# Kernel optimization log

Hardware: AMD Instinct MI355X
Metric: run time of the kernel (lower is better)

## Reference

```python
import jax, jax.numpy as jnp
import numpy as np

B, S, H = 8, 2048, 512
M = 4096
TEMP = 0.1
EPS = 1e-6


def setup_inputs() -> dict:
    key = jax.random.key(0)
    ks = jax.random.split(key, 8)
    scale = 1.0 / np.sqrt(H)
    return {
        "hidden_states": jax.random.normal(ks[0], (B, S, H), dtype=jnp.float32),
        "memory_keys": jax.random.normal(ks[1], (M, H), dtype=jnp.float32),
        "memory_values": jax.random.normal(ks[2], (M, H), dtype=jnp.float32),
        "Wk": jax.random.normal(ks[3], (H, H), dtype=jnp.float32) * scale,
        "bk": jnp.zeros((H,), dtype=jnp.float32),
        "Wo": jax.random.normal(ks[4], (H, H), dtype=jnp.float32) * scale,
        "bo": jnp.zeros((H,), dtype=jnp.float32),
        "memory_usage": jax.random.randint(ks[5], (M,), 0, 2, dtype=jnp.int32),
    }


def reference(hidden_states, memory_keys, memory_values, Wk, bk, Wo, bo, memory_usage):
    # key projection: [B,S,H]
    q = jnp.einsum("bsh,kh->bsk", hidden_states, Wk) + bk
    # L2-style normalization with eps inside rsqrt (matches torch.rsqrt(norm_sq + 1e-6))
    q_n = q * jax.lax.rsqrt(jnp.sum(q * q, axis=-1, keepdims=True) + EPS)
    mk_n = memory_keys * jax.lax.rsqrt(
        jnp.sum(memory_keys * memory_keys, axis=-1, keepdims=True) + EPS
    )
    # cosine-similarity scores over the memory bank: [B,S,M]
    scores = jnp.einsum("bsk,mk->bsm", q_n, mk_n) / TEMP
    mask = (memory_usage > 0).astype(scores.dtype)  # [M]
    scores = scores * mask + (-1e9) * (1.0 - mask)
    attn = jax.nn.softmax(scores, axis=-1)  # [B,S,M]
    retrieved = jnp.einsum("bsm,mv->bsv", attn, memory_values)  # [B,S,H]
    out = jnp.einsum("bsv,hv->bsh", retrieved, Wo) + bo
    return out
```

## Files before the change

### kernel.cpp

```cpp
#include <hip/hip_runtime.h>
#include <cstdint>
#include <cstddef>

#define H_DIM   512
#define M_DIM   4096

typedef unsigned short u16;
typedef short bf16x8 __attribute__((ext_vector_type(8)));
typedef float f32x4  __attribute__((ext_vector_type(4)));

__device__ __forceinline__ u16 f2b(float f) {
  union { float f; uint32_t u; } v; v.f = f;
  uint32_t u = v.u + (0x7FFFu + ((v.u >> 16) & 1u));
  return (u16)(u >> 16);
}

__device__ __forceinline__ bf16x8 cvt8(const float4& lo, const float4& hi) {
  union { u16 u[8]; bf16x8 v; } o;
  o.u[0] = f2b(lo.x); o.u[1] = f2b(lo.y); o.u[2] = f2b(lo.z); o.u[3] = f2b(lo.w);
  o.u[4] = f2b(hi.x); o.u[5] = f2b(hi.y); o.u[6] = f2b(hi.z); o.u[7] = f2b(hi.w);
  return o.v;
}

__global__ void k_f2bf_ww(const float* __restrict__ wk, const float* __restrict__ wo,
                          u16* __restrict__ owk, u16* __restrict__ owo) {
  int i = blockIdx.x * blockDim.x + threadIdx.x;
  const float* src = (i < 65536) ? wk : wo;
  u16* dst = (i < 65536) ? owk : owo;
  int j = i & 65535;
  float4 v = ((const float4*)src)[j];
  ushort4 o;
  o.x = f2b(v.x); o.y = f2b(v.y); o.z = f2b(v.z); o.w = f2b(v.w);
  ((ushort4*)dst)[j] = o;
}

__global__ void k_compact(const int* __restrict__ usage, int* __restrict__ idx,
                          int* __restrict__ meta) {
  __shared__ int cnt[256];
  int t = threadIdx.x;
  int base = t * 16;
  int c = 0;
  #pragma unroll
  for (int i = 0; i < 16; ++i) c += (usage[base + i] > 0) ? 1 : 0;
  cnt[t] = c;
  __syncthreads();
  for (int d = 1; d < 256; d <<= 1) {
    int v = (t >= d) ? cnt[t - d] : 0;
    __syncthreads();
    cnt[t] += v;
    __syncthreads();
  }
  int pos = cnt[t] - c;
  for (int i = 0; i < 16; ++i)
    if (usage[base + i] > 0) idx[pos++] = base + i;
  if (t == 0) {
    int total = cnt[255];
    int keff = ((total + 127) >> 7) << 7;
    meta[0] = total; meta[1] = keff; meta[2] = keff >> 5; meta[3] = keff >> 7;
  }
}

__global__ void k_gather_keys(const float* __restrict__ keys,
                              const int* __restrict__ idx, const int* __restrict__ meta,
                              u16* __restrict__ okeys) {
  int j    = blockIdx.x * 4 + (threadIdx.x >> 6);
  int lane = threadIdx.x & 63;
  int count = meta[0];
  ushort4* kp = (ushort4*)(okeys + (size_t)j * H_DIM);
  if (j >= count) {
    ushort4 z = {0, 0, 0, 0};
    kp[lane] = z; kp[lane + 64] = z;
    return;
  }
  int src = idx[j];
  const float4* rp = (const float4*)(keys + (size_t)src * H_DIM);
  float4 a = rp[lane];
  float4 b = rp[lane + 64];
  float ss = a.x*a.x + a.y*a.y + a.z*a.z + a.w*a.w
           + b.x*b.x + b.y*b.y + b.z*b.z + b.w*b.w;
  #pragma unroll
  for (int d = 1; d < 64; d <<= 1) ss += __shfl_xor(ss, d, 64);
  float s = rsqrtf(ss + 1e-6f);
  ushort4 oa, ob;
  oa.x = f2b(a.x*s); oa.y = f2b(a.y*s); oa.z = f2b(a.z*s); oa.w = f2b(a.w*s);
  ob.x = f2b(b.x*s); ob.y = f2b(b.y*s); ob.z = f2b(b.z*s); ob.w = f2b(b.w*s);
  kp[lane]      = oa;
  kp[lane + 64] = ob;
}

__global__ void k_reduce_l(const float* __restrict__ lpart, float* __restrict__ linv,
                           const int* __restrict__ meta) {
  int r = blockIdx.x * blockDim.x + threadIdx.x;
  int n = meta[1] >> 6;
  float s = 0.0f;
  for (int i = 0; i < n; ++i) s += lpart[(size_t)r * 64 + i];
  linv[r] = 1.0f / s;
}

__global__ __launch_bounds__(256, 3)
void k_gemm_mw(const u16* __restrict__ A, const float* __restrict__ Bf,
               const int* __restrict__ idx, const int* __restrict__ meta,
               u16* __restrict__ outh) {
  __shared__ u16 Ah[2][128 * 32];
  __shared__ u16 Bh[2][128 * 32];

  const int tid  = threadIdx.x;
  const int wave = tid >> 6, lane = tid & 63;
  const int wr = (wave >> 1) * 64;
  const int wc = (wave & 1) * 64;

  const int count = meta[0];
  if (blockIdx.x >= (meta[1] >> 7)) return;
  const int row0 = blockIdx.y << 7;
  const int col0 = blockIdx.x << 7;
  const int kiters = 512 >> 5;

  const int srow   = lane & 15;
  const int schunk = lane >> 4;
  const int lds_off = schunk * 128 + srow * 8;

  const int fr = lane & 15;
  const int fbase = (lane >> 4) * 128 + fr * 8;
  const int g = lane >> 4;

  const char* Ac = (const char*)A;

  uint32_t aB[2];
  uint32_t bB[2];
  bool bval[2];
  #pragma unroll
  for (int s2 = 0; s2 < 2; ++s2) {
    aB[s2] = (uint32_t)(((size_t)(row0 + (wave + s2 * 4) * 16 + srow) * 512u
                         + (size_t)(schunk * 8)) * 2u);
    int mrow = col0 + (wave + s2 * 4) * 16 + srow;
    bval[s2] = (mrow < count);
    int src = bval[s2] ? idx[mrow] : 0;
    bB[s2] = (uint32_t)(((size_t)src * 512u + (size_t)(schunk * 8)) * 4u);
  }

  f32x4 acc[4][4];
  const f32x4 z = {0.0f, 0.0f, 0.0f, 0.0f};
  #pragma unroll
  for (int i = 0; i < 4; ++i)
    #pragma unroll
    for (int j = 0; j < 4; ++j) acc[i][j] = z;

  bf16x8 rA[2];
  float4 rBlo[2], rBhi[2];
  auto gload = [&](int k0) {
    const uint32_t kb  = (uint32_t)(k0 << 1);
    const uint32_t kbf = (uint32_t)(k0 << 2);
    #pragma unroll
    for (int s2 = 0; s2 < 2; ++s2) rA[s2] = *(const bf16x8*)(Ac + aB[s2] + kb);
    #pragma unroll
    for (int s2 = 0; s2 < 2; ++s2) {
      rBlo[s2] = *(const float4*)((const char*)Bf + bB[s2] + kbf);
      rBhi[s2] = *(const float4*)((const char*)Bf + bB[s2] + kbf + 16);
    }
  };

  const float4 zf = {0.f, 0.f, 0.f, 0.f};
  gload(0);
  for (int it = 0; it < kiters; ++it) {
    const int cur = it & 1;
    #pragma unroll
    for (int s2 = 0; s2 < 2; ++s2)
      *(bf16x8*)&Ah[cur][(wave + s2 * 4) * 512 + lds_off] = rA[s2];
    #pragma unroll
    for (int s2 = 0; s2 < 2; ++s2)
      *(bf16x8*)&Bh[cur][(wave + s2 * 4) * 512 + lds_off] =
          bval[s2] ? cvt8(rBlo[s2], rBhi[s2]) : cvt8(zf, zf);
    if (it + 1 < kiters) gload((it + 1) << 5);
    __syncthreads();

    bf16x8 af[4], bfv[4];
    #pragma unroll
    for (int i = 0; i < 4; ++i)
      af[i] = *(const bf16x8*)&Ah[cur][((wr >> 4) + i) * 512 + fbase];
    #pragma unroll
    for (int j = 0; j < 4; ++j)
      bfv[j] = *(const bf16x8*)&Bh[cur][((wc >> 4) + j) * 512 + fbase];
    #pragma unroll
    for (int i = 0; i < 4; ++i)
      #pragma unroll
      for (int j = 0; j < 4; ++j)
        acc[i][j] = __builtin_amdgcn_mfma_f32_16x16x32_bf16(af[i], bfv[j], acc[i][j], 0, 0, 0);
  }

  #pragma unroll
  for (int i = 0; i < 4; ++i) {
    #pragma unroll
    for (int r = 0; r < 4; ++r) {
      int grow = row0 + wr + i * 16 + g * 4 + r;
      #pragma unroll
      for (int j = 0; j < 4; ++j) {
        int gcol = col0 + wc + j * 16 + fr;
        outh[(size_t)grow * (size_t)M_DIM + gcol] = f2b(acc[i][j][r]);
      }
    }
  }
}

#define EPI2_P     0
#define EPI2_OUT   1
#define EPI2_QPROJ 2

template<int EPI>
__global__ __launch_bounds__(512, 2)
void k_gemm2(const u16* __restrict__ A, const u16* __restrict__ B,
             const int* __restrict__ meta,
             float* __restrict__ outf, u16* __restrict__ outh,
             const float* __restrict__ bias,
             float* __restrict__ aux,
             const float* __restrict__ rowscale) {
  constexpr int BM   = (EPI == EPI2_P) ? 256 : 128;
  constexpr int MF   = BM / 32;
  constexpr int NF   = 4;
  constexpr int APS  = BM / 128;
  constexpr int NLA  = BM / 64;
  constexpr int NLB  = 4;
  constexpr int ASUB = BM * 32;
  constexpr int BSUB = 256 * 32;
  constexpr bool BF32 = (EPI == EPI2_QPROJ);

  __shared__ u16 Ah[2][BM * 64];
  __shared__ u16 Bh[2][256 * 64];

  const int tid  = threadIdx.x;
  const int wave = tid >> 6, lane = tid & 63;
  const int wave_m = wave >> 2, wave_n = wave & 3;
  const int wm0 = wave_m * (BM >> 1);
  const int wn0 = wave_n * 64;
  const int fr  = lane & 15, g = lane >> 4;
  const int fbase = g * 128 + fr * 8;

  int m0, r0, kel;
  if (EPI == EPI2_P) {
    int id = blockIdx.x + (blockIdx.y << 4);
    int xcd = id & 7, s = id >> 3;
    r0 = (xcd * 8 + (s >> 4)) << 8;
    m0 = (s & 15) << 8;
    if (m0 >= meta[1]) return;
    kel = 512;
  } else if (EPI == EPI2_OUT) {
    int id = blockIdx.x + (blockIdx.y << 2);
    int xcd = id & 7, s = id >> 3;
    r0 = (xcd * 8 + (s >> 2)) << 8;
    m0 = (s & 3) << 7;
    kel = meta[1];
  } else {
    int id = blockIdx.x + (blockIdx.y << 2);
    int xcd = id & 7, s = id >> 3;
    r0 = (xcd * 8 + (s >> 2)) << 8;
    m0 = (s & 3) << 7;
    kel = 512;
  }
  const int kiters = kel >> 6;
  if (kiters <= 0) return;
  const int kstr = (EPI == EPI2_OUT) ? M_DIM : 512;

  const char* Ac = (const char*)A;
  const char* Bc = (const char*)B;
  uint32_t aB[NLA], bB[NLB];
  #pragma unroll
  for (int s2 = 0; s2 < NLA; ++s2) {
    int ks = s2 / APS;
    int u  = tid + (s2 % APS) * 512;
    int row = ((u >> 6) << 4) + (u & 15);
    int kch = (u >> 4) & 3;
    aB[s2] = (uint32_t)(((size_t)(m0 + row) * (size_t)kstr
                         + (size_t)(ks * 32 + kch * 8)) * 2u);
  }
  #pragma unroll
  for (int s2 = 0; s2 < NLB; ++s2) {
    int ks = s2 >> 1;
    int u  = tid + (s2 & 1) * 512;
    int row = ((u >> 6) << 4) + (u & 15);
    int kch = (u >> 4) & 3;
    bB[s2] = (uint32_t)(((size_t)(r0 + row) * (size_t)kstr
                         + (size_t)(ks * 32 + kch * 8)) * (BF32 ? 4u : 2u));
  }

  f32x4 acc[MF][NF];
  const f32x4 z = {0.0f, 0.0f, 0.0f, 0.0f};
  #pragma unroll
  for (int i = 0; i < MF; ++i)
    #pragma unroll
    for (int j = 0; j < NF; ++j) acc[i][j] = z;

  auto gloadA = [&](bf16x8 (&ra)[NLA], int it1) {
    const uint32_t kb = (uint32_t)(it1 << 7);
    #pragma unroll
    for (int s2 = 0; s2 < NLA; ++s2) ra[s2] = *(const bf16x8*)(Ac + aB[s2] + kb);
  };
  auto gloadBh = [&](bf16x8 (&rb)[NLB], int it1) {
    const uint32_t kb = (uint32_t)(it1 << 7);
    #pragma unroll
    for (int s2 = 0; s2 < NLB; ++s2) rb[s2] = *(const bf16x8*)(Bc + bB[s2] + kb);
  };
  auto gloadBf = [&](float4 (&lo)[NLB], float4 (&hi)[NLB], int it1) {
    const uint32_t kb = (uint32_t)(it1 << 8);
    #pragma unroll
    for (int s2 = 0; s2 < NLB; ++s2) {
      lo[s2] = *(const float4*)(Bc + bB[s2] + kb);
      hi[s2] = *(const float4*)(Bc + bB[s2] + kb + 16);
    }
  };
  auto commitA = [&](int cur, bf16x8 (&ra)[NLA]) {
    #pragma unroll
    for (int s2 = 0; s2 < NLA; ++s2)
      *(bf16x8*)&Ah[cur][(s2 / APS) * ASUB + (tid + (s2 % APS) * 512) * 8] = ra[s2];
  };
  auto commitBh = [&](int cur, bf16x8 (&rb)[NLB]) {
    #pragma unroll
    for (int s2 = 0; s2 < NLB; ++s2)
      *(bf16x8*)&Bh[cur][(s2 >> 1) * BSUB + (tid + (s2 & 1) * 512) * 8] = rb[s2];
  };
  auto commitBf = [&](int cur, float4 (&lo)[NLB], float4 (&hi)[NLB]) {
    #pragma unroll
    for (int s2 = 0; s2 < NLB; ++s2)
      *(bf16x8*)&Bh[cur][(s2 >> 1) * BSUB + (tid + (s2 & 1) * 512) * 8] =
          cvt8(lo[s2], hi[s2]);
  };
  auto compute = [&](int cur) {
    bf16x8 af[MF], bfv[NF];
    #pragma unroll
    for (int i = 0; i < MF; ++i)
      af[i] = *(const bf16x8*)&Ah[cur][((wm0 >> 4) + i) * 512 + fbase];
    #pragma unroll
    for (int j = 0; j < NF; ++j)
      bfv[j] = *(const bf16x8*)&Bh[cur][((wn0 >> 4) + j) * 512 + fbase];
    #pragma unroll
    for (int i = 0; i < MF; ++i)
      #pragma unroll
      for (int j = 0; j < NF; ++j)
        acc[i][j] = __builtin_amdgcn_mfma_f32_16x16x32_bf16(af[i], bfv[j], acc[i][j], 0, 0, 0);
    #pragma unroll
    for (int i = 0; i < MF; ++i)
      af[i] = *(const bf16x8*)&Ah[cur][ASUB + ((wm0 >> 4) + i) * 512 + fbase];
    #pragma unroll
    for (int j = 0; j < NF; ++j)
      bfv[j] = *(const bf16x8*)&Bh[cur][BSUB + ((wn0 >> 4) + j) * 512 + fbase];
    #pragma unroll
    for (int i = 0; i < MF; ++i)
      #pragma unroll
      for (int j = 0; j < NF; ++j)
        acc[i][j] = __builtin_amdgcn_mfma_f32_16x16x32_bf16(af[i], bfv[j], acc[i][j], 0, 0, 0);
  };

  if constexpr (EPI == EPI2_P) {
    bf16x8 rA[NLA], rB[NLB];
    gloadA(rA, 0); gloadBh(rB, 0);
    for (int it = 0; it < kiters; ++it) {
      const int cur = it & 1;
      commitA(cur, rA); commitBh(cur, rB);
      if (it + 1 < kiters) { gloadA(rA, it + 1); gloadBh(rB, it + 1); }
      __syncthreads();
      compute(cur);
    }
  } else if constexpr (!BF32) {
    bf16x8 a0[NLA], b0[NLB], a1[NLA], b1[NLB];
    gloadA(a0, 0); gloadBh(b0, 0);
    if (kiters > 1) { gloadA(a1, 1); gloadBh(b1, 1); }
    for (int it = 0; it < kiters; it += 2) {
      commitA(0, a0); commitBh(0, b0);
      if (it + 2 < kiters) { gloadA(a0, it + 2); gloadBh(b0, it + 2); }
      __syncthreads();
      compute(0);
      commitA(1, a1); commitBh(1, b1);
      if (it + 3 < kiters) { gloadA(a1, it + 3); gloadBh(b1, it + 3); }
      __syncthreads();
      compute(1);
    }
  } else {
    bf16x8 a0[NLA], a1[NLA];
    float4 b0lo[NLB], b0hi[NLB], b1lo[NLB], b1hi[NLB];
    gloadA(a0, 0); gloadBf(b0lo, b0hi, 0);
    if (kiters > 1) { gloadA(a1, 1); gloadBf(b1lo, b1hi, 1); }
    for (int it = 0; it < kiters; it += 2) {
      commitA(0, a0); commitBf(0, b0lo, b0hi);
      if (it + 2 < kiters) { gloadA(a0, it + 2); gloadBf(b0lo, b0hi, it + 2); }
      __syncthreads();
      compute(0);
      commitA(1, a1); commitBf(1, b1lo, b1hi);
      if (it + 3 < kiters) { gloadA(a1, it + 3); gloadBf(b1lo, b1hi, it + 3); }
      __syncthreads();
      compute(1);
    }
  }

  if (EPI == EPI2_P) {
    const int count = meta[0];
    float rq10[NF];
    #pragma unroll
    for (int j = 0; j < NF; ++j) {
      const size_t rr = (size_t)(r0 + wn0 + j * 16 + fr);
      float ssum = 0.0f;
      #pragma unroll
      for (int i = 0; i < 8; ++i) ssum += rowscale[rr * 8 + i];
      rq10[j] = rsqrtf(ssum + 1e-6f) * 10.0f;
    }
    float sj[NF] = {0.f, 0.f, 0.f, 0.f};
    #pragma unroll
    for (int i = 0; i < MF; ++i) {
      const int mb = m0 + wm0 + i * 16 + g * 4;
      #pragma unroll
      for (int j = 0; j < NF; ++j) {
        const size_t rr = (size_t)(r0 + wn0 + j * 16 + fr);
        float p0 = (mb + 0 < count) ? __expf(acc[i][j][0] * rq10[j]) : 0.0f;
        float p1 = (mb + 1 < count) ? __expf(acc[i][j][1] * rq10[j]) : 0.0f;
        float p2 = (mb + 2 < count) ? __expf(acc[i][j][2] * rq10[j]) : 0.0f;
        float p3 = (mb + 3 < count) ? __expf(acc[i][j][3] * rq10[j]) : 0.0f;
        ushort4 st; st.x = f2b(p0); st.y = f2b(p1); st.z = f2b(p2); st.w = f2b(p3);
        *(ushort4*)(outh + rr * M_DIM + mb) = st;
        sj[j] += (p0 + p1) + (p2 + p3);
      }
    }
    const int slot = (m0 + wm0) >> 6;
    #pragma unroll
    for (int j = 0; j < NF; ++j) {
      float s = sj[j];
      s += __shfl_xor(s, 16, 64);
      s += __shfl_xor(s, 32, 64);
      if (lane < 16) {
        const size_t rr = (size_t)(r0 + wn0 + j * 16 + lane);
        aux[rr * 64 + slot]     = s;
        aux[rr * 64 + slot + 1] = 0.0f;
      }
    }
  } else if (EPI == EPI2_OUT) {
    float scl[NF];
    #pragma unroll
    for (int j = 0; j < NF; ++j)
      scl[j] = rowscale[r0 + wn0 + j * 16 + fr];
    #pragma unroll
    for (int i = 0; i < MF; ++i) {
      const int hb = m0 + wm0 + i * 16 + g * 4;
      const float4 bv = *(const float4*)(bias + hb);
      #pragma unroll
      for (int j = 0; j < NF; ++j) {
        const size_t rr = (size_t)(r0 + wn0 + j * 16 + fr);
        float4 o;
        o.x = acc[i][j][0] * scl[j] + bv.x;
        o.y = acc[i][j][1] * scl[j] + bv.y;
        o.z = acc[i][j][2] * scl[j] + bv.z;
        o.w = acc[i][j][3] * scl[j] + bv.w;
        *(float4*)(outf + rr * H_DIM + hb) = o;
      }
    }
  } else {
    float sj[NF] = {0.f, 0.f, 0.f, 0.f};
    #pragma unroll
    for (int i = 0; i < MF; ++i) {
      const int kb = m0 + wm0 + i * 16 + g * 4;
      const float4 bkv = *(const float4*)(bias + kb);
      #pragma unroll
      for (int j = 0; j < NF; ++j) {
        const size_t rr = (size_t)(r0 + wn0 + j * 16 + fr);
        float v0 = acc[i][j][0] + bkv.x;
        float v1 = acc[i][j][1] + bkv.y;
        float v2 = acc[i][j][2] + bkv.z;
        float v3 = acc[i][j][3] + bkv.w;
        ushort4 st; st.x = f2b(v0); st.y = f2b(v1); st.z = f2b(v2); st.w = f2b(v3);
        *(ushort4*)(outh + rr * H_DIM + kb) = st;
        sj[j] += v0 * v0 + v1 * v1 + v2 * v2 + v3 * v3;
      }
    }
    const int slot = (m0 + wm0) >> 6;
    #pragma unroll
    for (int j = 0; j < NF; ++j) {
      float s = sj[j];
      s += __shfl_xor(s, 16, 64);
      s += __shfl_xor(s, 32, 64);
      if (lane < 16)
        aux[(size_t)(r0 + wn0 + j * 16 + lane) * 8 + slot] = s;
    }
  }
}

extern "C" void kernel_launch(void* const* d_in, const int* in_sizes, int n_in,
                              void* d_out, int out_size, void* d_ws, size_t ws_size,
                              hipStream_t stream) {
  const float* hidden = (const float*)d_in[0];
  const float* mkeys  = (const float*)d_in[1];
  const float* mvals  = (const float*)d_in[2];
  const float* Wk     = (const float*)d_in[3];
  const float* bk     = (const float*)d_in[4];
  const float* Wo     = (const float*)d_in[5];
  const float* bo     = (const float*)d_in[6];
  const int*   usage  = (const int*)d_in[7];
  (void)in_sizes; (void)n_in; (void)out_size; (void)ws_size;

  char* ws = (char*)d_ws;
  int*   idx   = (int*)(ws + 0);
  int*   meta  = (int*)(ws + 16384);
  float* lpart = (float*)(ws + 1048576);
  float* qss   = (float*)(ws + 5242880);
  u16*   wkb   = (u16*)(ws + 16777216);
  u16*   wob   = (u16*)(ws + 17301504);
  u16*   mkn   = (u16*)(ws + 17825792);
  u16*   qb    = (u16*)(ws + 26214400);
  u16*   MWt   = (u16*)(ws + 42991616);
  u16*   P     = (u16*)(ws + 47185920);
  float* linv  = (float*)(ws + 183828480);

  k_f2bf_ww<<<512, 256, 0, stream>>>(Wk, Wo, wkb, wob);

  k_compact<<<1, 256, 0, stream>>>(usage, idx, meta);
  k_gather_keys<<<1024, 256, 0, stream>>>(mkeys, idx, meta, mkn);

  k_gemm2<EPI2_QPROJ><<<dim3(4, 64), 512, 0, stream>>>(wkb, (const u16*)hidden,
      nullptr, nullptr, qb, bk, qss, nullptr);

  k_gemm_mw<<<dim3(16, 4), 256, 0, stream>>>(wob, mvals, idx, meta, MWt);

  k_gemm2<EPI2_P><<<dim3(16, 64), 512, 0, stream>>>(mkn, qb, meta,
      nullptr, P, nullptr, lpart, qss);
  k_reduce_l<<<64, 256, 0, stream>>>(lpart, linv, meta);

  k_gemm2<EPI2_OUT><<<dim3(4, 64), 512, 0, stream>>>(MWt, P, meta,
      (float*)d_out, nullptr, bo, nullptr, linv);
}
```

Measured before the change: 252.5 us.

## Split Q-projection kernel out and triple-buffer the bf16 GEMMs with phased MFMA scheduling

Moves the fp32-input Q projection into its own dedicated kernel. The scores GEMM and the output GEMM now use a three-stage LDS ring with K-steps of 32 instead of 64. Each K-step is split into two MFMA halves separated by barriers, and global loads and LDS commits are interleaved between those halves. The MFMA sections are wrapped in raised s_setprio. The goal is to overlap memory latency with matrix work and cut the LDS footprint per stage. The cost is more barriers per K-iteration and more complex buffer-index logic.

```diff
diff --git a/kernel.cpp b/kernel.cpp
--- a/kernel.cpp
+++ b/kernel.cpp
@@ -201,30 +201,175 @@
   }
 }
 
-#define EPI2_P     0
-#define EPI2_OUT   1
-#define EPI2_QPROJ 2
+__global__ __launch_bounds__(512, 2)
+void k_qproj(const u16* __restrict__ A, const float* __restrict__ Bf,
+             u16* __restrict__ outh, const float* __restrict__ bias,
+             float* __restrict__ aux) {
+  constexpr int NLA  = 2;
+  constexpr int NLB  = 4;
+  constexpr int ASUB = 128 * 32;
+  constexpr int BSUB = 256 * 32;
+
+  __shared__ u16 Ah[2][128 * 64];
+  __shared__ u16 Bh[2][256 * 64];
+
+  const int tid  = threadIdx.x;
+  const int wave = tid >> 6, lane = tid & 63;
+  const int wave_m = wave >> 2, wave_n = wave & 3;
+  const int wm0 = wave_m * 64;
+  const int wn0 = wave_n * 64;
+  const int fr  = lane & 15, g = lane >> 4;
+  const int fbase = g * 128 + fr * 8;
+
+  int id = blockIdx.x + (blockIdx.y << 2);
+  int xcd = id & 7, s = id >> 3;
+  const int r0 = (xcd * 8 + (s >> 2)) << 8;
+  const int m0 = (s & 3) << 7;
+  const int kiters = 512 >> 6;
+
+  const char* Ac = (const char*)A;
+  uint32_t aB[NLA], bB[NLB];
+  #pragma unroll
+  for (int s2 = 0; s2 < NLA; ++s2) {
+    int ks = s2;
+    int u  = tid;
+    int row = ((u >> 6) << 4) + (u & 15);
+    int kch = (u >> 4) & 3;
+    aB[s2] = (uint32_t)(((size_t)(m0 + row) * 512u
+                         + (size_t)(ks * 32 + kch * 8)) * 2u);
+  }
+  #pragma unroll
+  for (int s2 = 0; s2 < NLB; ++s2) {
+    int ks = s2 >> 1;
+    int u  = tid + (s2 & 1) * 512;
+    int row = ((u >> 6) << 4) + (u & 15);
+    int kch = (u >> 4) & 3;
+    bB[s2] = (uint32_t)(((size_t)(r0 + row) * 512u
+                         + (size_t)(ks * 32 + kch * 8)) * 4u);
+  }
+
+  f32x4 acc[4][4];
+  const f32x4 z = {0.0f, 0.0f, 0.0f, 0.0f};
+  #pragma unroll
+  for (int i = 0; i < 4; ++i)
+    #pragma unroll
+    for (int j = 0; j < 4; ++j) acc[i][j] = z;
+
+  auto gloadA = [&](bf16x8 (&ra)[NLA], int it1) {
+    const uint32_t kb = (uint32_t)(it1 << 7);
+    #pragma unroll
+    for (int s2 = 0; s2 < NLA; ++s2) ra[s2] = *(const bf16x8*)(Ac + aB[s2] + kb);
+  };
+  auto gloadBf = [&](float4 (&lo)[NLB], float4 (&hi)[NLB], int it1) {
+    const uint32_t kb = (uint32_t)(it1 << 8);
+    #pragma unroll
+    for (int s2 = 0; s2 < NLB; ++s2) {
+      lo[s2] = *(const float4*)((const char*)Bf + bB[s2] + kb);
+      hi[s2] = *(const float4*)((const char*)Bf + bB[s2] + kb + 16);
+    }
+  };
+  auto commitA = [&](int cur, bf16x8 (&ra)[NLA]) {
+    #pragma unroll
+    for (int s2 = 0; s2 < NLA; ++s2)
+      *(bf16x8*)&Ah[cur][s2 * ASUB + tid * 8] = ra[s2];
+  };
+  auto commitBf = [&](int cur, float4 (&lo)[NLB], float4 (&hi)[NLB]) {
+    #pragma unroll
+    for (int s2 = 0; s2 < NLB; ++s2)
+      *(bf16x8*)&Bh[cur][(s2 >> 1) * BSUB + (tid + (s2 & 1) * 512) * 8] =
+          cvt8(lo[s2], hi[s2]);
+  };
+  auto compute = [&](int cur) {
+    bf16x8 af[4], bfv[4];
+    #pragma unroll
+    for (int i = 0; i < 4; ++i)
+      af[i] = *(const bf16x8*)&Ah[cur][((wm0 >> 4) + i) * 512 + fbase];
+    #pragma unroll
+    for (int j = 0; j < 4; ++j)
+      bfv[j] = *(const bf16x8*)&Bh[cur][((wn0 >> 4) + j) * 512 + fbase];
+    #pragma unroll
+    for (int i = 0; i < 4; ++i)
+      #pragma unroll
+      for (int j = 0; j < 4; ++j)
+        acc[i][j] = __builtin_amdgcn_mfma_f32_16x16x32_bf16(af[i], bfv[j], acc[i][j], 0, 0, 0);
+    #pragma unroll
+    for (int i = 0; i < 4; ++i)
+      af[i] = *(const bf16x8*)&Ah[cur][ASUB + ((wm0 >> 4) + i) * 512 + fbase];
+    #pragma unroll
+    for (int j = 0; j < 4; ++j)
+      bfv[j] = *(const bf16x8*)&Bh[cur][BSUB + ((wn0 >> 4) + j) * 512 + fbase];
+    #pragma unroll
+    for (int i = 0; i < 4; ++i)
+      #pragma unroll
+      for (int j = 0; j < 4; ++j)
+        acc[i][j] = __builtin_amdgcn_mfma_f32_16x16x32_bf16(af[i], bfv[j], acc[i][j], 0, 0, 0);
+  };
+
+  bf16x8 a0[NLA], a1[NLA];
+  float4 b0lo[NLB], b0hi[NLB], b1lo[NLB], b1hi[NLB];
+  gloadA(a0, 0); gloadBf(b0lo, b0hi, 0);
+  gloadA(a1, 1); gloadBf(b1lo, b1hi, 1);
+  for (int it = 0; it < kiters; it += 2) {
+    commitA(0, a0); commitBf(0, b0lo, b0hi);
+    if (it + 2 < kiters) { gloadA(a0, it + 2); gloadBf(b0lo, b0hi, it + 2); }
+    __syncthreads();
+    compute(0);
+    commitA(1, a1); commitBf(1, b1lo, b1hi);
+    if (it + 3 < kiters) { gloadA(a1, it + 3); gloadBf(b1lo, b1hi, it + 3); }
+    __syncthreads();
+    compute(1);
+  }
+
+  float sj[4] = {0.f, 0.f, 0.f, 0.f};
+  #pragma unroll
+  for (int i = 0; i < 4; ++i) {
+    const int kb = m0 + wm0 + i * 16 + g * 4;
+    const float4 bkv = *(const float4*)(bias + kb);
+    #pragma unroll
+    for (int j = 0; j < 4; ++j) {
+      const size_t rr = (size_t)(r0 + wn0 + j * 16 + fr);
+      float v0 = acc[i][j][0] + bkv.x;
+      float v1 = acc[i][j][1] + bkv.y;
+      float v2 = acc[i][j][2] + bkv.z;
+      float v3 = acc[i][j][3] + bkv.w;
+      ushort4 st; st.x = f2b(v0); st.y = f2b(v1); st.z = f2b(v2); st.w = f2b(v3);
+      *(ushort4*)(outh + rr * H_DIM + kb) = st;
+      sj[j] += v0 * v0 + v1 * v1 + v2 * v2 + v3 * v3;
+    }
+  }
+  const int slot = (m0 + wm0) >> 6;
+  #pragma unroll
+  for (int j = 0; j < 4; ++j) {
+    float s2 = sj[j];
+    s2 += __shfl_xor(s2, 16, 64);
+    s2 += __shfl_xor(s2, 32, 64);
+    if (lane < 16)
+      aux[(size_t)(r0 + wn0 + j * 16 + lane) * 8 + slot] = s2;
+  }
+}
+
+#define EPI3_P   0
+#define EPI3_OUT 1
 
 template<int EPI>
 __global__ __launch_bounds__(512, 2)
-void k_gemm2(const u16* __restrict__ A, const u16* __restrict__ B,
+void k_gemm3(const u16* __restrict__ A, const u16* __restrict__ B,
              const int* __restrict__ meta,
              float* __restrict__ outf, u16* __restrict__ outh,
              const float* __restrict__ bias,
              float* __restrict__ aux,
              const float* __restrict__ rowscale) {
-  constexpr int BM   = (EPI == EPI2_P) ? 256 : 128;
+  constexpr int BM   = (EPI == EPI3_P) ? 256 : 128;
   constexpr int MF   = BM / 32;
+  constexpr int MH   = MF / 2;
   constexpr int NF   = 4;
-  constexpr int APS  = BM / 128;
-  constexpr int NLA  = BM / 64;
-  constexpr int NLB  = 4;
-  constexpr int ASUB = BM * 32;
-  constexpr int BSUB = 256 * 32;
-  constexpr bool BF32 = (EPI == EPI2_QPROJ);
-
-  __shared__ u16 Ah[2][BM * 64];
-  __shared__ u16 Bh[2][256 * 64];
+  constexpr int NLA  = BM / 128;
+  constexpr int NLB  = 2;
+  constexpr int AT   = BM * 32;
+  constexpr int BT   = 256 * 32;
+
+  __shared__ u16 Ah[3][AT];
+  __shared__ u16 Bh[3][BT];
 
   const int tid  = threadIdx.x;
   const int wave = tid >> 6, lane = tid & 63;
@@ -235,50 +380,41 @@
   const int fbase = g * 128 + fr * 8;
 
   int m0, r0, kel;
-  if (EPI == EPI2_P) {
+  if (EPI == EPI3_P) {
     int id = blockIdx.x + (blockIdx.y << 4);
     int xcd = id & 7, s = id >> 3;
     r0 = (xcd * 8 + (s >> 4)) << 8;
     m0 = (s & 15) << 8;
     if (m0 >= meta[1]) return;
     kel = 512;
-  } else if (EPI == EPI2_OUT) {
+  } else {
     int id = blockIdx.x + (blockIdx.y << 2);
     int xcd = id & 7, s = id >> 3;
     r0 = (xcd * 8 + (s >> 2)) << 8;
     m0 = (s & 3) << 7;
     kel = meta[1];
-  } else {
-    int id = blockIdx.x + (blockIdx.y << 2);
-    int xcd = id & 7, s = id >> 3;
-    r0 = (xcd * 8 + (s >> 2)) << 8;
-    m0 = (s & 3) << 7;
-    kel = 512;
-  }
-  const int kiters = kel >> 6;
-  if (kiters <= 0) return;
-  const int kstr = (EPI == EPI2_OUT) ? M_DIM : 512;
+  }
+  const int kiters = kel >> 5;
+  const int kstr = (EPI == EPI3_OUT) ? M_DIM : 512;
 
   const char* Ac = (const char*)A;
   const char* Bc = (const char*)B;
   uint32_t aB[NLA], bB[NLB];
   #pragma unroll
   for (int s2 = 0; s2 < NLA; ++s2) {
-    int ks = s2 / APS;
-    int u  = tid + (s2 % APS) * 512;
+    int u  = tid + s2 * 512;
     int row = ((u >> 6) << 4) + (u & 15);
     int kch = (u >> 4) & 3;
     aB[s2] = (uint32_t)(((size_t)(m0 + row) * (size_t)kstr
-                         + (size_t)(ks * 32 + kch * 8)) * 2u);
+                         + (size_t)(kch * 8)) * 2u);
   }
   #pragma unroll
   for (int s2 = 0; s2 < NLB; ++s2) {
-    int ks = s2 >> 1;
-    int u  = tid + (s2 & 1) * 512;
+    int u  = tid + s2 * 512;
     int row = ((u >> 6) << 4) + (u & 15);
     int kch = (u >> 4) & 3;
     bB[s2] = (uint32_t)(((size_t)(r0 + row) * (size_t)kstr
-                         + (size_t)(ks * 32 + kch * 8)) * (BF32 ? 4u : 2u));
+                         + (size_t)(kch * 8)) * 2u);
   }
 
   f32x4 acc[MF][NF];
@@ -288,108 +424,95 @@
     #pragma unroll
     for (int j = 0; j < NF; ++j) acc[i][j] = z;
 
-  auto gloadA = [&](bf16x8 (&ra)[NLA], int it1) {
-    const uint32_t kb = (uint32_t)(it1 << 7);
-    #pragma unroll
-    for (int s2 = 0; s2 < NLA; ++s2) ra[s2] = *(const bf16x8*)(Ac + aB[s2] + kb);
-  };
-  auto gloadBh = [&](bf16x8 (&rb)[NLB], int it1) {
-    const uint32_t kb = (uint32_t)(it1 << 7);
-    #pragma unroll
-    for (int s2 = 0; s2 < NLB; ++s2) rb[s2] = *(const bf16x8*)(Bc + bB[s2] + kb);
-  };
-  auto gloadBf = [&](float4 (&lo)[NLB], float4 (&hi)[NLB], int it1) {
-    const uint32_t kb = (uint32_t)(it1 << 8);
-    #pragma unroll
-    for (int s2 = 0; s2 < NLB; ++s2) {
-      lo[s2] = *(const float4*)(Bc + bB[s2] + kb);
-      hi[s2] = *(const float4*)(Bc + bB[s2] + kb + 16);
-    }
-  };
-  auto commitA = [&](int cur, bf16x8 (&ra)[NLA]) {
+  bf16x8 g0a[NLA], g0b[NLB], g1a[NLA], g1b[NLB];
+
+  auto gload = [&](bf16x8 (&ga)[NLA], bf16x8 (&gb)[NLB], int t) {
+    const uint32_t kb = (uint32_t)(t << 6);
+    #pragma unroll
+    for (int s2 = 0; s2 < NLA; ++s2) ga[s2] = *(const bf16x8*)(Ac + aB[s2] + kb);
+    #pragma unroll
+    for (int s2 = 0; s2 < NLB; ++s2) gb[s2] = *(const bf16x8*)(Bc + bB[s2] + kb);
+  };
+  auto commit = [&](int buf, bf16x8 (&ga)[NLA], bf16x8 (&gb)[NLB]) {
     #pragma unroll
     for (int s2 = 0; s2 < NLA; ++s2)
-      *(bf16x8*)&Ah[cur][(s2 / APS) * ASUB + (tid + (s2 % APS) * 512) * 8] = ra[s2];
-  };
-  auto commitBh = [&](int cur, bf16x8 (&rb)[NLB]) {
+      *(bf16x8*)&Ah[buf][(tid + s2 * 512) * 8] = ga[s2];
     #pragma unroll
     for (int s2 = 0; s2 < NLB; ++s2)
-      *(bf16x8*)&Bh[cur][(s2 >> 1) * BSUB + (tid + (s2 & 1) * 512) * 8] = rb[s2];
-  };
-  auto commitBf = [&](int cur, float4 (&lo)[NLB], float4 (&hi)[NLB]) {
-    #pragma unroll
-    for (int s2 = 0; s2 < NLB; ++s2)
-      *(bf16x8*)&Bh[cur][(s2 >> 1) * BSUB + (tid + (s2 & 1) * 512) * 8] =
-          cvt8(lo[s2], hi[s2]);
-  };
-  auto compute = [&](int cur) {
-    bf16x8 af[MF], bfv[NF];
-    #pragma unroll
-    for (int i = 0; i < MF; ++i)
-      af[i] = *(const bf16x8*)&Ah[cur][((wm0 >> 4) + i) * 512 + fbase];
+      *(bf16x8*)&Bh[buf][(tid + s2 * 512) * 8] = gb[s2];
+  };
+
+  bf16x8 af[MF], bfv[NF];
+
+  #define PHASE_SYNC() do {                                   \
+    __builtin_amdgcn_s_barrier();                             \
+    asm volatile("s_waitcnt lgkmcnt(0)" ::: "memory");        \
+    __builtin_amdgcn_sched_barrier(0);                        \
+  } while (0)
+
+  #define MFMA_HALF(base) do {                                \
+    __builtin_amdgcn_s_setprio(1);                            \
+    _Pragma("unroll")                                         \
+    for (int i = 0; i < MH; ++i)                              \
+      _Pragma("unroll")                                       \
+      for (int j = 0; j < NF; ++j)                            \
+        acc[(base) + i][j] = __builtin_amdgcn_mfma_f32_16x16x32_bf16( \
+            af[(base) + i], bfv[j], acc[(base) + i][j], 0, 0, 0);    \
+    __builtin_amdgcn_s_setprio(0);                            \
+    __builtin_amdgcn_s_barrier();                             \
+  } while (0)
+
+  gload(g0a, g0b, 0);
+  commit(0, g0a, g0b);
+  gload(g1a, g1b, 1);
+  asm volatile("s_waitcnt lgkmcnt(0)" ::: "memory");
+  __builtin_amdgcn_s_barrier();
+
+  int bc = 0;
+  for (int it = 0; it < kiters; it += 2) {
+    const int b0i = bc;
+    const int b1i = (bc + 1 == 3) ? 0 : bc + 1;
+    const int b2i = (bc + 2 >= 3) ? bc - 1 : bc + 2;
+
+    #pragma unroll
+    for (int i = 0; i < MH; ++i)
+      af[i] = *(const bf16x8*)&Ah[b0i][((wm0 >> 4) + i) * 512 + fbase];
     #pragma unroll
     for (int j = 0; j < NF; ++j)
-      bfv[j] = *(const bf16x8*)&Bh[cur][((wn0 >> 4) + j) * 512 + fbase];
-    #pragma unroll
-    for (int i = 0; i < MF; ++i)
-      #pragma unroll
-      for (int j = 0; j < NF; ++j)
-        acc[i][j] = __builtin_amdgcn_mfma_f32_16x16x32_bf16(af[i], bfv[j], acc[i][j], 0, 0, 0);
-    #pragma unroll
-    for (int i = 0; i < MF; ++i)
-      af[i] = *(const bf16x8*)&Ah[cur][ASUB + ((wm0 >> 4) + i) * 512 + fbase];
+      bfv[j] = *(const bf16x8*)&Bh[b0i][((wn0 >> 4) + j) * 512 + fbase];
+    if (it + 2 < kiters) gload(g0a, g0b, it + 2);
+    PHASE_SYNC();
+    MFMA_HALF(0);
+    #pragma unroll
+    for (int i = 0; i < MH; ++i)
+      af[MH + i] = *(const bf16x8*)&Ah[b0i][((wm0 >> 4) + MH + i) * 512 + fbase];
+    if (it + 1 < kiters) commit(b1i, g1a, g1b);
+    PHASE_SYNC();
+    MFMA_HALF(MH);
+
+    #pragma unroll
+    for (int i = 0; i < MH; ++i)
+      af[i] = *(const bf16x8*)&Ah[b1i][((wm0 >> 4) + i) * 512 + fbase];
     #pragma unroll
     for (int j = 0; j < NF; ++j)
-      bfv[j] = *(const bf16x8*)&Bh[cur][BSUB + ((wn0 >> 4) + j) * 512 + fbase];
-    #pragma unroll
-    for (int i = 0; i < MF; ++i)
-      #pragma unroll
-      for (int j = 0; j < NF; ++j)
-        acc[i][j] = __builtin_amdgcn_mfma_f32_16x16x32_bf16(af[i], bfv[j], acc[i][j], 0, 0, 0);
-  };
-
-  if constexpr (EPI == EPI2_P) {
-    bf16x8 rA[NLA], rB[NLB];
-    gloadA(rA, 0); gloadBh(rB, 0);
-    for (int it = 0; it < kiters; ++it) {
-      const int cur = it & 1;
-      commitA(cur, rA); commitBh(cur, rB);
-      if (it + 1 < kiters) { gloadA(rA, it + 1); gloadBh(rB, it + 1); }
-      __syncthreads();
-      compute(cur);
-    }
-  } else if constexpr (!BF32) {
-    bf16x8 a0[NLA], b0[NLB], a1[NLA], b1[NLB];
-    gloadA(a0, 0); gloadBh(b0, 0);
-    if (kiters > 1) { gloadA(a1, 1); gloadBh(b1, 1); }
-    for (int it = 0; it < kiters; it += 2) {
-      commitA(0, a0); commitBh(0, b0);
-      if (it + 2 < kiters) { gloadA(a0, it + 2); gloadBh(b0, it + 2); }
-      __syncthreads();
-      compute(0);
-      commitA(1, a1); commitBh(1, b1);
-      if (it + 3 < kiters) { gloadA(a1, it + 3); gloadBh(b1, it + 3); }
-      __syncthreads();
-      compute(1);
-    }
-  } else {
-    bf16x8 a0[NLA], a1[NLA];
-    float4 b0lo[NLB], b0hi[NLB], b1lo[NLB], b1hi[NLB];
-    gloadA(a0, 0); gloadBf(b0lo, b0hi, 0);
-    if (kiters > 1) { gloadA(a1, 1); gloadBf(b1lo, b1hi, 1); }
-    for (int it = 0; it < kiters; it += 2) {
-      commitA(0, a0); commitBf(0, b0lo, b0hi);
-      if (it + 2 < kiters) { gloadA(a0, it + 2); gloadBf(b0lo, b0hi, it + 2); }
-      __syncthreads();
-      compute(0);
-      commitA(1, a1); commitBf(1, b1lo, b1hi);
-      if (it + 3 < kiters) { gloadA(a1, it + 3); gloadBf(b1lo, b1hi, it + 3); }
-      __syncthreads();
-      compute(1);
-    }
-  }
-
-  if (EPI == EPI2_P) {
+      bfv[j] = *(const bf16x8*)&Bh[b1i][((wn0 >> 4) + j) * 512 + fbase];
+    if (it + 3 < kiters) gload(g1a, g1b, it + 3);
+    PHASE_SYNC();
+    MFMA_HALF(0);
+    #pragma unroll
+    for (int i = 0; i < MH; ++i)
+      af[MH + i] = *(const bf16x8*)&Ah[b1i][((wm0 >> 4) + MH + i) * 512 + fbase];
+    if (it + 2 < kiters) commit(b2i, g0a, g0b);
+    PHASE_SYNC();
+    MFMA_HALF(MH);
+
+    bc = (bc + 2 >= 3) ? bc - 1 : bc + 2;
+  }
+
+  #undef PHASE_SYNC
+  #undef MFMA_HALF
+
+  if (EPI == EPI3_P) {
     const int count = meta[0];
     float rq10[NF];
     #pragma unroll
@@ -428,7 +551,7 @@
         aux[rr * 64 + slot + 1] = 0.0f;
       }
     }
-  } else if (EPI == EPI2_OUT) {
+  } else {
     float scl[NF];
     #pragma unroll
     for (int j = 0; j < NF; ++j)
@@ -448,33 +571,6 @@
         *(float4*)(outf + rr * H_DIM + hb) = o;
       }
     }
-  } else {
-    float sj[NF] = {0.f, 0.f, 0.f, 0.f};
-    #pragma unroll
-    for (int i = 0; i < MF; ++i) {
-      const int kb = m0 + wm0 + i * 16 + g * 4;
-      const float4 bkv = *(const float4*)(bias + kb);
-      #pragma unroll
-      for (int j = 0; j < NF; ++j) {
-        const size_t rr = (size_t)(r0 + wn0 + j * 16 + fr);
-        float v0 = acc[i][j][0] + bkv.x;
-        float v1 = acc[i][j][1] + bkv.y;
-        float v2 = acc[i][j][2] + bkv.z;
-        float v3 = acc[i][j][3] + bkv.w;
-        ushort4 st; st.x = f2b(v0); st.y = f2b(v1); st.z = f2b(v2); st.w = f2b(v3);
-        *(ushort4*)(outh + rr * H_DIM + kb) = st;
-        sj[j] += v0 * v0 + v1 * v1 + v2 * v2 + v3 * v3;
-      }
-    }
-    const int slot = (m0 + wm0) >> 6;
-    #pragma unroll
-    for (int j = 0; j < NF; ++j) {
-      float s = sj[j];
-      s += __shfl_xor(s, 16, 64);
-      s += __shfl_xor(s, 32, 64);
-      if (lane < 16)
-        aux[(size_t)(r0 + wn0 + j * 16 + lane) * 8 + slot] = s;
-    }
   }
 }
 
@@ -509,15 +605,14 @@
   k_compact<<<1, 256, 0, stream>>>(usage, idx, meta);
   k_gather_keys<<<1024, 256, 0, stream>>>(mkeys, idx, meta, mkn);
 
-  k_gemm2<EPI2_QPROJ><<<dim3(4, 64), 512, 0, stream>>>(wkb, (const u16*)hidden,
-      nullptr, nullptr, qb, bk, qss, nullptr);
+  k_qproj<<<dim3(4, 64), 512, 0, stream>>>(wkb, hidden, qb, bk, qss);
 
   k_gemm_mw<<<dim3(16, 4), 256, 0, stream>>>(wob, mvals, idx, meta, MWt);
 
-  k_gemm2<EPI2_P><<<dim3(16, 64), 512, 0, stream>>>(mkn, qb, meta,
+  k_gemm3<EPI3_P><<<dim3(16, 64), 512, 0, stream>>>(mkn, qb, meta,
       nullptr, P, nullptr, lpart, qss);
   k_reduce_l<<<64, 256, 0, stream>>>(lpart, linv, meta);
 
-  k_gemm2<EPI2_OUT><<<dim3(4, 64), 512, 0, stream>>>(MWt, P, meta,
+  k_gemm3<EPI3_OUT><<<dim3(4, 64), 512, 0, stream>>>(MWt, P, meta,
       (float*)d_out, nullptr, bo, nullptr, linv);
 }
```

After: 274.4 us. 1.09x slower.
